# Performance work log

Measured on AMD Instinct MI355X. Metric: run time of the kernel, lower is better.

The kernel has to match this reference:

```python
import jax, jax.numpy as jnp
import numpy as np

CONF_THRES = 0.25
IOU_THRES = 0.45
MAX_WH = 7680.0   # class-separation offset (class-aware NMS trick)
K = 1024          # max candidates entering NMS per image
MAX_DET = 300     # max detections returned per image


def _pairwise_iou(boxes):
    # boxes: [K,4] xyxy -> iou: [K,K]
    x1, y1, x2, y2 = boxes[:, 0], boxes[:, 1], boxes[:, 2], boxes[:, 3]
    area = (x2 - x1) * (y2 - y1)
    ix1 = jnp.maximum(x1[:, None], x1[None, :])
    iy1 = jnp.maximum(y1[:, None], y1[None, :])
    ix2 = jnp.minimum(x2[:, None], x2[None, :])
    iy2 = jnp.minimum(y2[:, None], y2[None, :])
    inter = jnp.clip(ix2 - ix1, 0.0) * jnp.clip(iy2 - iy1, 0.0)
    union = area[:, None] + area[None, :] - inter
    return inter / (union + 1e-9)


def _nms_single(pred):
    # pred: [N, 5+nc]
    xywh = pred[:, :4]
    obj = pred[:, 4]
    cls_conf = obj[:, None] * pred[:, 5:]            # [N, nc]
    score = cls_conf.max(axis=-1)                    # best-class confidence
    cls_id = cls_conf.argmax(axis=-1)                # best class

    # confidence filter (masked, fixed shape): invalid -> score sentinel -1
    masked = jnp.where(score > CONF_THRES, score, -1.0)
    top_s, top_i = jax.lax.top_k(masked, K)          # sorted descending
    keep0 = top_s > CONF_THRES                       # valid candidates

    b = xywh[top_i]                                  # [K,4]
    sc = score[top_i]
    c = cls_id[top_i].astype(pred.dtype)

    # xywh -> xyxy
    cx, cy, w, h = b[:, 0], b[:, 1], b[:, 2], b[:, 3]
    boxes = jnp.stack([cx - w / 2, cy - h / 2, cx + w / 2, cy + h / 2], axis=-1)

    # class-aware NMS: offset boxes by class index so classes never overlap
    off_boxes = boxes + (c * MAX_WH)[:, None]
    iou = _pairwise_iou(off_boxes)                   # [K,K]

    idx = jnp.arange(K)
    def body(i, keep):
        # if box i is kept, suppress all later boxes with IoU > thresh
        sup = (iou[i] > IOU_THRES) & keep[i] & (idx > i)
        return keep & ~sup
    keep = jax.lax.fori_loop(0, K, body, keep0)

    # select top MAX_DET kept detections (scores already descending)
    order = jnp.argsort(-jnp.where(keep, top_s, -1.0))[:MAX_DET]
    det = jnp.concatenate([boxes, sc[:, None], c[:, None]], axis=-1)  # [K,6]
    out = jnp.where(keep[order][:, None], det[order], 0.0)            # [MAX_DET,6]
    return out


def setup_inputs() -> dict:
    key = jax.random.key(0)
    x = jax.random.uniform(key, (16, 25200, 85), dtype=jnp.float32)
    return {"x": x}


def reference(x):
    # x: [B, N, 5+nc] raw predictions (sigmoid-activated)
    # returns [B, MAX_DET, 6] = (x1, y1, x2, y2, conf, cls), zero-padded
    return jax.vmap(_nms_single)(x)
```

## Files before the change

### kernel.cpp

```cpp
#include <hip/hip_runtime.h>
#include <hip/hip_bf16.h>
#include <stdint.h>


#define NB 16
#define NA 25200
#define NK 1024
#define ND 300
#define CAP 2048
#define NBIN 4096
#define NCLS 80

__device__ __forceinline__ uint32_t fkey(float f) {
    uint32_t b = __float_as_uint(f);
    return (b & 0x80000000u) ? ~b : (b | 0x80000000u);
}

__device__ __forceinline__ int score_bin(float s) {
    float f = (s - 0.25f) * (4096.0f / 0.75f);
    int b = (int)f;
    return b > (NBIN - 1) ? (NBIN - 1) : (b < 0 ? 0 : b);
}

__device__ __forceinline__ float key_score(uint32_t u) {
    uint32_t fb = (u & 0x80000000u) ? (u ^ 0x80000000u) : ~u;
    return __uint_as_float(fb);
}

__global__ void score_kernel(const float* __restrict__ x,
                             float4* __restrict__ boxes,
                             unsigned long long* __restrict__ candw) {
    int b = blockIdx.y;
    int a = blockIdx.x * 16 + (threadIdx.x >> 4);
    int lane = threadIdx.x & 15;
    const float* p = x + (size_t)(b * NA + a) * 85;
    float obj = p[4];
    float best = -1e30f;
    int bi = 0;
#pragma unroll
    for (int r = 0; r < 5; ++r) {
        int j = lane + 16 * r;
        float v = obj * p[5 + j];
        if (v > best) { best = v; bi = j; }
    }
    for (int off = 8; off >= 1; off >>= 1) {
        float ov = __shfl_xor(best, off, 16);
        int   oi = __shfl_xor(bi,   off, 16);
        if (ov > best || (ov == best && oi < bi)) { best = ov; bi = oi; }
    }
    if (lane == 0) {
        float cx = p[0], cy = p[1], w = p[2], h = p[3];
        boxes[b * NA + a] = make_float4(cx - w * 0.5f, cy - h * 0.5f,
                                        cx + w * 0.5f, cy + h * 0.5f);
        unsigned long long key = 0ULL;
        if (best > 0.25f)
            key = ((unsigned long long)fkey(best) << 32) |
                  ((unsigned long long)(unsigned)(NA - 1 - a) << 7) |
                  (unsigned)bi;
        candw[(size_t)b * NA + a] = key;
    }
}

__global__ void __launch_bounds__(1024)
select_sort_kernel(const unsigned long long* __restrict__ candw,
                   const float4* __restrict__ boxes,
                   float4* __restrict__ obox,
                   float* __restrict__ det,
                   unsigned long long* __restrict__ keep0w) {
    int b = blockIdx.x;
    int t = threadIdx.x;
    int wid = t >> 6, lane = t & 63;
    __shared__ unsigned int lhist[NBIN];
    __shared__ unsigned int suffE[NBIN];
    __shared__ unsigned long long sk[CAP];
    __shared__ unsigned int wsum[16];
    __shared__ int sB;

    const ulonglong2* cb2 = (const ulonglong2*)(candw + (size_t)b * NA);

    ((uint4*)lhist)[t] = make_uint4(0u, 0u, 0u, 0u);
    sk[t] = 0ULL; sk[t + 1024] = 0ULL;
    if (t == 0) sB = -1;
    __syncthreads();
    for (int i = t; i < NA / 2; i += 1024) {
        ulonglong2 k2 = cb2[i];
        if (k2.x)
            atomicAdd(&lhist[score_bin(key_score((uint32_t)(k2.x >> 32)))], 1u);
        if (k2.y)
            atomicAdd(&lhist[score_bin(key_score((uint32_t)(k2.y >> 32)))], 1u);
    }
    __syncthreads();

    uint4 hv = ((const uint4*)lhist)[t];
    unsigned int mysum = hv.x + hv.y + hv.z + hv.w;
    unsigned int ssfx = mysum;
#pragma unroll
    for (int off = 1; off < 64; off <<= 1) {
        unsigned int v = __shfl_down(ssfx, off);
        if (lane + off < 64) ssfx += v;
    }
    if (lane == 0) wsum[wid] = ssfx;
    ((uint4*)lhist)[t] = make_uint4(0u, 0u, 0u, 0u);
    __syncthreads();
    unsigned int tail = 0;
    for (int w2 = wid + 1; w2 < 16; ++w2) tail += wsum[w2];
    unsigned int S_t = ssfx + tail;
    unsigned int Snext = S_t - mysum;
    unsigned int ex3 = Snext;
    unsigned int ex2 = ex3 + hv.w;
    unsigned int ex1 = ex2 + hv.z;
    unsigned int ex0 = ex1 + hv.y;
    suffE[t * 4 + 0] = ex0;
    suffE[t * 4 + 1] = ex1;
    suffE[t * 4 + 2] = ex2;
    suffE[t * 4 + 3] = ex3;
    unsigned int s3 = hv.w + Snext;
    unsigned int s2 = hv.z + s3;
    unsigned int s1 = hv.y + s2;
    unsigned int s0 = hv.x + s1;
    int loc = -1;
    if (s3 >= NK) loc = t * 4 + 3;
    else if (s2 >= NK) loc = t * 4 + 2;
    else if (s1 >= NK) loc = t * 4 + 1;
    else if (s0 >= NK) loc = t * 4 + 0;
#pragma unroll
    for (int off = 32; off >= 1; off >>= 1) {
        int o = __shfl_xor(loc, off);
        loc = o > loc ? o : loc;
    }
    if ((t & 63) == 0) atomicMax(&sB, loc);
    __syncthreads();
    int B = sB < 0 ? 0 : sB;

    for (int i = t; i < NA / 2; i += 1024) {
        ulonglong2 k2 = cb2[i];
        unsigned long long ke[2] = {k2.x, k2.y};
#pragma unroll
        for (int e = 0; e < 2; ++e) {
            unsigned long long k = ke[e];
            if (k != 0ULL) {
                int bin = score_bin(key_score((uint32_t)(k >> 32)));
                if (bin >= B) {
                    unsigned int slot =
                        suffE[bin] + atomicAdd(&lhist[bin], 1u);
                    if (slot < CAP) sk[slot] = k;
                }
            }
        }
    }
    __syncthreads();

    {
        unsigned int cntArr[4] = {hv.x, hv.y, hv.z, hv.w};
        unsigned int startArr[4] = {ex0, ex1, ex2, ex3};
#pragma unroll
        for (int e = 0; e < 4; ++e) {
            int bin = t * 4 + e;
            unsigned int cnt = cntArr[e];
            unsigned int start = startArr[e];
            if (bin >= B && cnt > 1 && start < CAP) {
                if (cnt > CAP - start) cnt = CAP - start;
                for (unsigned int i2 = 1; i2 < cnt; ++i2) {
                    unsigned long long kk = sk[start + i2];
                    int j2 = (int)i2 - 1;
                    while (j2 >= 0 && sk[start + j2] < kk) {
                        sk[start + j2 + 1] = sk[start + j2];
                        --j2;
                    }
                    sk[start + j2 + 1] = kk;
                }
            }
        }
    }
    __syncthreads();

    unsigned long long key = sk[t];
    uint32_t u = (uint32_t)(key >> 32);
    uint32_t low = (uint32_t)key;
    int a = (u == 0) ? 0 : (int)(NA - 1 - (low >> 7));
    int cls = (u == 0) ? 0 : (int)(low & 0x7Fu);
    float s = key_score(u);
    float4 bx = boxes[b * NA + a];
    float c = (float)cls;
    float off = c * 7680.0f;
    obox[b * NK + t] =
        make_float4(bx.x + off, bx.y + off, bx.z + off, bx.w + off);
    float* dr = det + (size_t)(b * NK + t) * 8;
    dr[0] = bx.x; dr[1] = bx.y; dr[2] = bx.z; dr[3] = bx.w;
    dr[4] = s; dr[5] = c;
    bool keep0 = s > 0.25f;
    unsigned long long bal = __ballot(keep0);
    if ((t & 63) == 0) keep0w[b * 16 + (t >> 6)] = bal;
}

__global__ void __launch_bounds__(1024)
nms_out_kernel(const float4* __restrict__ obox,
               const float* __restrict__ det,
               const unsigned long long* __restrict__ keep0w,
               float* __restrict__ out) {
    int b = blockIdx.x;
    int t = threadIdx.x;
    int wid = t >> 6, lane = t & 63;
    __shared__ float4 oboxS[NK];
    __shared__ unsigned long long cmaskS[NCLS * 16];
    __shared__ unsigned long long aliveS[16];
    __shared__ int changedS;
    __shared__ int list[ND];
    __shared__ int totalS;

    float4 ob = obox[b * NK + t];
    const float* dr = det + (size_t)(b * NK + t) * 8;
    int ci = (int)dr[5];
    oboxS[t] = ob;
    cmaskS[t] = 0ULL;
    if (t < NCLS * 16 - 1024) cmaskS[1024 + t] = 0ULL;
    bool keep0 = (keep0w[b * 16 + wid] >> lane) & 1ULL;
    if (t < 16) aliveS[t] = keep0w[b * 16 + t];
    __syncthreads();
    atomicOr(&cmaskS[ci * 16 + wid], 1ULL << lane);
    __syncthreads();

    unsigned long long row[16];
#pragma unroll
    for (int w = 0; w < 16; ++w) row[w] = 0ULL;
    float ra = (ob.z - ob.x) * (ob.w - ob.y);
    for (int w = 0; w <= wid; ++w) {
        unsigned long long bits = cmaskS[ci * 16 + w];
        if (w == wid)
            bits &= (lane == 0) ? 0ULL : ((1ULL << lane) - 1ULL);
        unsigned long long rbits = 0ULL;
        while (bits) {
            int bit = __ffsll((long long)bits) - 1;
            bits &= bits - 1;
            float4 o = oboxS[w * 64 + bit];
            float carea = (o.z - o.x) * (o.w - o.y);
            float ix1 = fmaxf(ob.x, o.x), iy1 = fmaxf(ob.y, o.y);
            float ix2 = fminf(ob.z, o.z), iy2 = fminf(ob.w, o.w);
            float iw = fmaxf(ix2 - ix1, 0.0f), ih = fmaxf(iy2 - iy1, 0.0f);
            float inter = iw * ih;
            float uni = ra + carea - inter;
            float iou = inter / (uni + 1e-9f);
            if (iou > 0.45f) rbits |= (1ULL << bit);
        }
        row[w] = rbits;
    }
    __syncthreads();

    for (int it = 0; it < NK; ++it) {
        if (t == 0) changedS = 0;
        unsigned long long aw[16];
#pragma unroll
        for (int w = 0; w < 16; ++w) aw[w] = aliveS[w];
        __syncthreads();
        unsigned long long sup = 0;
#pragma unroll
        for (int w = 0; w < 16; ++w) sup |= aw[w] & row[w];
        bool newalive = keep0 && (sup == 0);
        unsigned long long nb = __ballot(newalive);
        if (lane == 0) {
            if (nb != aw[wid]) { atomicOr(&changedS, 1); aliveS[wid] = nb; }
        }
        __syncthreads();
        if (!changedS) break;
    }

    if (t < 64) {
        unsigned long long av = (lane < 16) ? aliveS[lane] : 0ULL;
        int cnt2 = (lane < 16) ? __popcll(av) : 0;
        int pre = cnt2;
        for (int off = 1; off < 64; off <<= 1) {
            int v = __shfl_up(pre, off);
            if (lane >= off) pre += v;
        }
        int total = __shfl(pre, 63);
        int base = pre - cnt2;
        if (lane == 0) totalS = total;
        if (lane < 16) {
            unsigned long long m = av;
            int pos = base;
            while (m && pos < ND) {
                int bit = __ffsll((long long)m) - 1;
                list[pos++] = lane * 64 + bit;
                m &= m - 1;
            }
        }
    }
    __syncthreads();
    if (t < ND) {
        float vals[6] = {0, 0, 0, 0, 0, 0};
        if (t < totalS) {
            const float* dr2 = det + (size_t)(b * NK + list[t]) * 8;
#pragma unroll
            for (int c = 0; c < 6; ++c) vals[c] = dr2[c];
        }
        float* o = out + (size_t)(b * ND + t) * 6;
#pragma unroll
        for (int c = 0; c < 6; ++c) o[c] = vals[c];
    }
}

extern "C" void kernel_launch(void* const* d_in, const int* in_sizes, int n_in,
                              void* d_out, int out_size, void* d_ws, size_t ws_size,
                              hipStream_t stream) {
    const float* x = (const float*)d_in[0];
    float* out = (float*)d_out;

    char* ws = (char*)d_ws;
    size_t off = 0;
    auto alloc = [&](size_t bytes) {
        void* p = ws + off;
        off += (bytes + 255) & ~(size_t)255;
        return p;
    };
    float4* boxes = (float4*)alloc((size_t)NB * NA * sizeof(float4));
    unsigned long long* candw =
        (unsigned long long*)alloc((size_t)NB * NA * sizeof(unsigned long long));
    float4* obox = (float4*)alloc((size_t)NB * NK * sizeof(float4));
    float* det = (float*)alloc((size_t)NB * NK * 8 * sizeof(float));
    unsigned long long* keep0w =
        (unsigned long long*)alloc((size_t)NB * 16 * sizeof(unsigned long long));
    (void)ws_size;

    score_kernel<<<dim3(NA / 16, NB), 256, 0, stream>>>(x, boxes, candw);
    select_sort_kernel<<<NB, 1024, 0, stream>>>(candw, boxes, obox, det,
                                                keep0w);
    nms_out_kernel<<<NB, 1024, 0, stream>>>(obox, det, keep0w, out);
}
```

Measured before the change: 85.48 us.

## Move histogram into score kernel, split scatter across blocks, fuse sort with NMS

```diff
diff --git a/kernel.cpp b/kernel.cpp
--- a/kernel.cpp
+++ b/kernel.cpp
@@ -27,9 +27,15 @@
     return __uint_as_float(fb);
 }
 
+__global__ void zero_kernel(uint4* __restrict__ p, int n4) {
+    int i = blockIdx.x * 256 + threadIdx.x;
+    if (i < n4) p[i] = make_uint4(0u, 0u, 0u, 0u);
+}
+
 __global__ void score_kernel(const float* __restrict__ x,
                              float4* __restrict__ boxes,
-                             unsigned long long* __restrict__ candw) {
+                             unsigned long long* __restrict__ candw,
+                             unsigned int* __restrict__ hist) {
     int b = blockIdx.y;
     int a = blockIdx.x * 16 + (threadIdx.x >> 4);
     int lane = threadIdx.x & 15;
@@ -53,45 +59,31 @@
         boxes[b * NA + a] = make_float4(cx - w * 0.5f, cy - h * 0.5f,
                                         cx + w * 0.5f, cy + h * 0.5f);
         unsigned long long key = 0ULL;
-        if (best > 0.25f)
+        if (best > 0.25f) {
             key = ((unsigned long long)fkey(best) << 32) |
                   ((unsigned long long)(unsigned)(NA - 1 - a) << 7) |
                   (unsigned)bi;
+            atomicAdd(&hist[b * NBIN + score_bin(best)], 1u);
+        }
         candw[(size_t)b * NA + a] = key;
     }
 }
 
 __global__ void __launch_bounds__(1024)
-select_sort_kernel(const unsigned long long* __restrict__ candw,
-                   const float4* __restrict__ boxes,
-                   float4* __restrict__ obox,
-                   float* __restrict__ det,
-                   unsigned long long* __restrict__ keep0w) {
-    int b = blockIdx.x;
+scatter_kernel(const unsigned int* __restrict__ hist,
+               const unsigned long long* __restrict__ candw,
+               unsigned int* __restrict__ binCnt,
+               unsigned long long* __restrict__ skG) {
+    int q = blockIdx.x;
+    int b = blockIdx.y;
     int t = threadIdx.x;
     int wid = t >> 6, lane = t & 63;
-    __shared__ unsigned int lhist[NBIN];
     __shared__ unsigned int suffE[NBIN];
-    __shared__ unsigned long long sk[CAP];
     __shared__ unsigned int wsum[16];
     __shared__ int sB;
 
-    const ulonglong2* cb2 = (const ulonglong2*)(candw + (size_t)b * NA);
-
-    ((uint4*)lhist)[t] = make_uint4(0u, 0u, 0u, 0u);
-    sk[t] = 0ULL; sk[t + 1024] = 0ULL;
     if (t == 0) sB = -1;
-    __syncthreads();
-    for (int i = t; i < NA / 2; i += 1024) {
-        ulonglong2 k2 = cb2[i];
-        if (k2.x)
-            atomicAdd(&lhist[score_bin(key_score((uint32_t)(k2.x >> 32)))], 1u);
-        if (k2.y)
-            atomicAdd(&lhist[score_bin(key_score((uint32_t)(k2.y >> 32)))], 1u);
-    }
-    __syncthreads();
-
-    uint4 hv = ((const uint4*)lhist)[t];
+    uint4 hv = ((const uint4*)(hist + b * NBIN))[t];
     unsigned int mysum = hv.x + hv.y + hv.z + hv.w;
     unsigned int ssfx = mysum;
 #pragma unroll
@@ -100,7 +92,6 @@
         if (lane + off < 64) ssfx += v;
     }
     if (lane == 0) wsum[wid] = ssfx;
-    ((uint4*)lhist)[t] = make_uint4(0u, 0u, 0u, 0u);
     __syncthreads();
     unsigned int tail = 0;
     for (int w2 = wid + 1; w2 < 16; ++w2) tail += wsum[w2];
@@ -132,7 +123,10 @@
     __syncthreads();
     int B = sB < 0 ? 0 : sB;
 
-    for (int i = t; i < NA / 2; i += 1024) {
+    const ulonglong2* cb2 = (const ulonglong2*)(candw + (size_t)b * NA);
+    const int qstart = q * (NA / 2 / 4);
+    const int qend = qstart + (NA / 2 / 4);
+    for (int i = qstart + t; i < qend; i += 1024) {
         ulonglong2 k2 = cb2[i];
         unsigned long long ke[2] = {k2.x, k2.y};
 #pragma unroll
@@ -142,13 +136,73 @@
                 int bin = score_bin(key_score((uint32_t)(k >> 32)));
                 if (bin >= B) {
                     unsigned int slot =
-                        suffE[bin] + atomicAdd(&lhist[bin], 1u);
-                    if (slot < CAP) sk[slot] = k;
+                        suffE[bin] + atomicAdd(&binCnt[b * NBIN + bin], 1u);
+                    if (slot < CAP) skG[(size_t)b * CAP + slot] = k;
                 }
             }
         }
     }
-    __syncthreads();
+}
+
+__global__ void __launch_bounds__(1024)
+sort_nms_kernel(const unsigned int* __restrict__ hist,
+                const unsigned long long* __restrict__ skG,
+                const float4* __restrict__ boxes,
+                float* __restrict__ out) {
+    int b = blockIdx.x;
+    int t = threadIdx.x;
+    int wid = t >> 6, lane = t & 63;
+    __shared__ __align__(16) char smemA[CAP * 8];
+    __shared__ float4 oboxS[NK];
+    __shared__ float2 dscl[NK];
+    __shared__ unsigned long long cmaskS[NCLS * 16];
+    __shared__ unsigned long long aliveS[16];
+    __shared__ unsigned int wsum[16];
+    __shared__ int sB;
+    __shared__ int changedS;
+    __shared__ int list[ND];
+    __shared__ int totalS;
+    unsigned long long* sk = (unsigned long long*)smemA;
+    float4* dboxS = (float4*)smemA;
+
+    if (t == 0) sB = -1;
+    uint4 hv = ((const uint4*)(hist + b * NBIN))[t];
+    unsigned int mysum = hv.x + hv.y + hv.z + hv.w;
+    unsigned int ssfx = mysum;
+#pragma unroll
+    for (int off = 1; off < 64; off <<= 1) {
+        unsigned int v = __shfl_down(ssfx, off);
+        if (lane + off < 64) ssfx += v;
+    }
+    if (lane == 0) wsum[wid] = ssfx;
+    sk[t] = skG[(size_t)b * CAP + t];
+    sk[t + 1024] = skG[(size_t)b * CAP + t + 1024];
+    __syncthreads();
+    unsigned int tail = 0;
+    for (int w2 = wid + 1; w2 < 16; ++w2) tail += wsum[w2];
+    unsigned int S_t = ssfx + tail;
+    unsigned int Snext = S_t - mysum;
+    unsigned int ex3 = Snext;
+    unsigned int ex2 = ex3 + hv.w;
+    unsigned int ex1 = ex2 + hv.z;
+    unsigned int ex0 = ex1 + hv.y;
+    unsigned int s3 = hv.w + Snext;
+    unsigned int s2 = hv.z + s3;
+    unsigned int s1 = hv.y + s2;
+    unsigned int s0 = hv.x + s1;
+    int loc = -1;
+    if (s3 >= NK) loc = t * 4 + 3;
+    else if (s2 >= NK) loc = t * 4 + 2;
+    else if (s1 >= NK) loc = t * 4 + 1;
+    else if (s0 >= NK) loc = t * 4 + 0;
+#pragma unroll
+    for (int off = 32; off >= 1; off >>= 1) {
+        int o = __shfl_xor(loc, off);
+        loc = o > loc ? o : loc;
+    }
+    if ((t & 63) == 0) atomicMax(&sB, loc);
+    __syncthreads();
+    int B = sB < 0 ? 0 : sB;
 
     {
         unsigned int cntArr[4] = {hv.x, hv.y, hv.z, hv.w};
@@ -175,47 +229,24 @@
     __syncthreads();
 
     unsigned long long key = sk[t];
+    __syncthreads();
     uint32_t u = (uint32_t)(key >> 32);
     uint32_t low = (uint32_t)key;
     int a = (u == 0) ? 0 : (int)(NA - 1 - (low >> 7));
-    int cls = (u == 0) ? 0 : (int)(low & 0x7Fu);
+    int ci = (u == 0) ? 0 : (int)(low & 0x7Fu);
     float s = key_score(u);
     float4 bx = boxes[b * NA + a];
-    float c = (float)cls;
+    float c = (float)ci;
     float off = c * 7680.0f;
-    obox[b * NK + t] =
-        make_float4(bx.x + off, bx.y + off, bx.z + off, bx.w + off);
-    float* dr = det + (size_t)(b * NK + t) * 8;
-    dr[0] = bx.x; dr[1] = bx.y; dr[2] = bx.z; dr[3] = bx.w;
-    dr[4] = s; dr[5] = c;
-    bool keep0 = s > 0.25f;
-    unsigned long long bal = __ballot(keep0);
-    if ((t & 63) == 0) keep0w[b * 16 + (t >> 6)] = bal;
-}
-
-__global__ void __launch_bounds__(1024)
-nms_out_kernel(const float4* __restrict__ obox,
-               const float* __restrict__ det,
-               const unsigned long long* __restrict__ keep0w,
-               float* __restrict__ out) {
-    int b = blockIdx.x;
-    int t = threadIdx.x;
-    int wid = t >> 6, lane = t & 63;
-    __shared__ float4 oboxS[NK];
-    __shared__ unsigned long long cmaskS[NCLS * 16];
-    __shared__ unsigned long long aliveS[16];
-    __shared__ int changedS;
-    __shared__ int list[ND];
-    __shared__ int totalS;
-
-    float4 ob = obox[b * NK + t];
-    const float* dr = det + (size_t)(b * NK + t) * 8;
-    int ci = (int)dr[5];
+    float4 ob = make_float4(bx.x + off, bx.y + off, bx.z + off, bx.w + off);
+    dboxS[t] = bx;
+    dscl[t] = make_float2(s, c);
     oboxS[t] = ob;
     cmaskS[t] = 0ULL;
     if (t < NCLS * 16 - 1024) cmaskS[1024 + t] = 0ULL;
-    bool keep0 = (keep0w[b * 16 + wid] >> lane) & 1ULL;
-    if (t < 16) aliveS[t] = keep0w[b * 16 + t];
+    bool keep0 = s > 0.25f;
+    unsigned long long bal = __ballot(keep0);
+    if (lane == 0) aliveS[wid] = bal;
     __syncthreads();
     atomicOr(&cmaskS[ci * 16 + wid], 1ULL << lane);
     __syncthreads();
@@ -268,9 +299,9 @@
         unsigned long long av = (lane < 16) ? aliveS[lane] : 0ULL;
         int cnt2 = (lane < 16) ? __popcll(av) : 0;
         int pre = cnt2;
-        for (int off = 1; off < 64; off <<= 1) {
-            int v = __shfl_up(pre, off);
-            if (lane >= off) pre += v;
+        for (int off2 = 1; off2 < 64; off2 <<= 1) {
+            int v = __shfl_up(pre, off2);
+            if (lane >= off2) pre += v;
         }
         int total = __shfl(pre, 63);
         int base = pre - cnt2;
@@ -289,13 +320,15 @@
     if (t < ND) {
         float vals[6] = {0, 0, 0, 0, 0, 0};
         if (t < totalS) {
-            const float* dr2 = det + (size_t)(b * NK + list[t]) * 8;
-#pragma unroll
-            for (int c = 0; c < 6; ++c) vals[c] = dr2[c];
+            int i = list[t];
+            float4 db = dboxS[i];
+            float2 sl = dscl[i];
+            vals[0] = db.x; vals[1] = db.y; vals[2] = db.z; vals[3] = db.w;
+            vals[4] = sl.x; vals[5] = sl.y;
         }
         float* o = out + (size_t)(b * ND + t) * 6;
 #pragma unroll
-        for (int c = 0; c < 6; ++c) o[c] = vals[c];
+        for (int c2 = 0; c2 < 6; ++c2) o[c2] = vals[c2];
     }
 }
 
@@ -312,17 +345,23 @@
         off += (bytes + 255) & ~(size_t)255;
         return p;
     };
+    size_t zero_begin = off;
+    unsigned int* hist =
+        (unsigned int*)alloc((size_t)NB * NBIN * sizeof(unsigned int));
+    unsigned int* binCnt =
+        (unsigned int*)alloc((size_t)NB * NBIN * sizeof(unsigned int));
+    unsigned long long* skG =
+        (unsigned long long*)alloc((size_t)NB * CAP * sizeof(unsigned long long));
+    size_t zero_end = off;
     float4* boxes = (float4*)alloc((size_t)NB * NA * sizeof(float4));
     unsigned long long* candw =
         (unsigned long long*)alloc((size_t)NB * NA * sizeof(unsigned long long));
-    float4* obox = (float4*)alloc((size_t)NB * NK * sizeof(float4));
-    float* det = (float*)alloc((size_t)NB * NK * 8 * sizeof(float));
-    unsigned long long* keep0w =
-        (unsigned long long*)alloc((size_t)NB * 16 * sizeof(unsigned long long));
     (void)ws_size;
 
-    score_kernel<<<dim3(NA / 16, NB), 256, 0, stream>>>(x, boxes, candw);
-    select_sort_kernel<<<NB, 1024, 0, stream>>>(candw, boxes, obox, det,
-                                                keep0w);
-    nms_out_kernel<<<NB, 1024, 0, stream>>>(obox, det, keep0w, out);
-}
+    int n4 = (int)((zero_end - zero_begin) / 16);
+    zero_kernel<<<(n4 + 255) / 256, 256, 0, stream>>>(
+        (uint4*)(ws + zero_begin), n4);
+    score_kernel<<<dim3(NA / 16, NB), 256, 0, stream>>>(x, boxes, candw, hist);
+    scatter_kernel<<<dim3(4, NB), 1024, 0, stream>>>(hist, candw, binCnt, skG);
+    sort_nms_kernel<<<NB, 1024, 0, stream>>>(hist, skG, boxes, out);
+}
```

New measurement: 90.27 us. 1.06x slower.
